# Performance work log

Hardware: AMD Instinct MI355X
Metric: run time of the kernel (lower is better)

The kernel has to match this reference:

```python
import jax, jax.numpy as jnp
import numpy as np

B, H, Q, N = 4, 32, 16, 4096
H_KV, D = 8, 128
N_KEEP = 3072
GROUPS = H // H_KV  # num_key_value_groups = 4


def setup_inputs() -> dict:
    key = jax.random.key(0)
    k1, k2, k3, k4 = jax.random.split(key, 4)
    attn_w = jax.random.uniform(k1, (B, H, Q, N), dtype=jnp.float32)
    # normalize to look like softmax output over the kv axis
    attn_w = attn_w / attn_w.sum(-1, keepdims=True)
    v_cache = jax.random.normal(k2, (B, H_KV, N, D), dtype=jnp.float32)
    o_proj_w = jax.random.normal(k3, (H * D, H * D), dtype=jnp.float32) * (1.0 / np.sqrt(H * D))
    keep_idx = jnp.sort(jax.random.randint(k4, (N_KEEP,), 0, N, dtype=jnp.int64))
    return {"attn_w": attn_w, "v_cache": v_cache, "o_proj_w": o_proj_w, "keep_idx": keep_idx}


def reference(attn_w, v_cache, o_proj_w, keep_idx):
    # 1) gather kept KV positions in the attention weights and renormalize
    aw = jnp.take(attn_w, keep_idx, axis=-1)              # [B,H,Q,Nk]
    aw = aw / (aw.sum(-1, keepdims=True) + 1e-6)
    # 2) gather kept V entries and repeat_kv across query-head groups
    v_new = jnp.take(v_cache, keep_idx, axis=2)           # [B,H_kv,Nk,D]
    v_all = jnp.repeat(v_new, GROUPS, axis=1)             # [B,H,Nk,D]
    # 3) recompute context and output projection
    ctx = jnp.einsum('bhqn,bhnd->bhqd', aw, v_all)        # [B,H,Q,D]
    ctx = ctx.transpose(0, 2, 1, 3).reshape(B, Q, H * D)  # [B,Q,H*D]
    out = ctx @ o_proj_w.T                                # nn.Linear: x @ W^T
    return out, aw
```

## Files before the change

### kernel.cpp

```cpp
#include <hip/hip_runtime.h>
#include <hip/hip_bf16.h>

#define BB   4
#define HH   32
#define QQ   16
#define NN   4096
#define HKV  8
#define DD   128
#define NK   3072
#define GRP  4

typedef __attribute__((ext_vector_type(8))) short bf16x8;
typedef __attribute__((ext_vector_type(4))) float f32x4;

__device__ __forceinline__ unsigned int pack_bf16(float lo, float hi) {
    union { unsigned int u; __hip_bfloat16 h[2]; } p;
    p.h[0] = __float2bfloat16(lo);
    p.h[1] = __float2bfloat16(hi);
    return p.u;
}

__global__ __launch_bounds__(256)
void k1_gather_norm(const float* __restrict__ attn_w,
                    const int* __restrict__ keep_idx,
                    float* __restrict__ aw_out)
{
    const int row = blockIdx.x;
    const float* src = attn_w + (size_t)row * NN;
    float* dst = aw_out + (size_t)row * NK;

    __shared__ float vals[NK];
    __shared__ float red[256];

    float s = 0.f;
    for (int k = threadIdx.x; k < NK; k += 256) {
        float v = src[keep_idx[k]];
        vals[k] = v;
        s += v;
    }
    red[threadIdx.x] = s;
    __syncthreads();
    for (int st = 128; st > 0; st >>= 1) {
        if (threadIdx.x < st) red[threadIdx.x] += red[threadIdx.x + st];
        __syncthreads();
    }
    const float inv = 1.0f / (red[0] + 1e-6f);
    for (int k = threadIdx.x; k < NK; k += 256)
        dst[k] = vals[k] * inv;
}

#define SPLITK2 16
#define KPB2    (NK / SPLITK2)
#define KCH     64

__global__ __launch_bounds__(256)
void k2_ctx(const float* __restrict__ aw,
            const float* __restrict__ v_cache,
            const int* __restrict__ keep_idx,
            __hip_bfloat16* __restrict__ partial)
{
    const int bid = blockIdx.x;
    const int ks  = bid & 15;
    const int hkv = (bid >> 4) & 7;
    const int b   = bid >> 7;
    const int tid = threadIdx.x;
    const int lane = tid & 63;
    const int w    = tid >> 6;
    const int fr   = lane & 15;
    const int kg   = lane >> 4;

    __shared__ unsigned short Vt[128 * 64];
    __shared__ int idxs[KCH];

    const int k0 = ks * KPB2;
    const float* arow = aw + (size_t)((b * HH + hkv * GRP + w) * QQ + fr) * NK + k0;
    const float* vb   = v_cache + (size_t)(b * HKV + hkv) * NN * DD;

    f32x4 acc[8];
#pragma unroll
    for (int nt = 0; nt < 8; ++nt) acc[nt] = (f32x4){0.f, 0.f, 0.f, 0.f};

    const int sd  = tid & 127;
    const int sc0 = tid >> 7;

    for (int c = 0; c < KPB2; c += KCH) {
        __syncthreads();
        if (tid < KCH) idxs[tid] = keep_idx[k0 + c + tid];
        __syncthreads();

#pragma unroll
        for (int p = 0; p < 4; ++p) {
            const int cs = sc0 + 2 * p;
            float v[8];
#pragma unroll
            for (int e = 0; e < 8; ++e)
                v[e] = vb[(size_t)idxs[8 * cs + e] * DD + sd];
            uint4 pk;
            pk.x = pack_bf16(v[0], v[1]);
            pk.y = pack_bf16(v[2], v[3]);
            pk.z = pack_bf16(v[4], v[5]);
            pk.w = pack_bf16(v[6], v[7]);
            const int us = sd * 64 + ((cs ^ (sd & 7)) << 3);
            *reinterpret_cast<uint4*>(&Vt[us]) = pk;
        }
        __syncthreads();

#pragma unroll
        for (int kc = 0; kc < 2; ++kc) {
            const float* ap = arow + c + kc * 32 + kg * 8;
            const float4 a0 = *reinterpret_cast<const float4*>(ap);
            const float4 a1 = *reinterpret_cast<const float4*>(ap + 4);
            union { bf16x8 v; unsigned int u[4]; } af;
            af.u[0] = pack_bf16(a0.x, a0.y);
            af.u[1] = pack_bf16(a0.z, a0.w);
            af.u[2] = pack_bf16(a1.x, a1.y);
            af.u[3] = pack_bf16(a1.z, a1.w);

            const int cs = kc * 4 + kg;
            const int xr = (cs ^ (fr & 7)) << 3;
#pragma unroll
            for (int nt = 0; nt < 8; ++nt) {
                const int d  = nt * 16 + fr;
                const int us = d * 64 + xr;
                bf16x8 bf = *reinterpret_cast<const bf16x8*>(&Vt[us]);
                acc[nt] = __builtin_amdgcn_mfma_f32_16x16x32_bf16(af.v, bf, acc[nt], 0, 0, 0);
            }
        }
    }

    __hip_bfloat16* pb = partial + (size_t)bid * (64 * DD);
#pragma unroll
    for (int nt = 0; nt < 8; ++nt) {
#pragma unroll
        for (int reg = 0; reg < 4; ++reg) {
            const int row = w * 16 + kg * 4 + reg;
            pb[row * DD + nt * 16 + fr] = __float2bfloat16(acc[nt][reg]);
        }
    }
}

__global__ __launch_bounds__(256)
void k3_reduce(const __hip_bfloat16* __restrict__ partial,
               __hip_bfloat16* __restrict__ ctxb)
{
    const int flat = blockIdx.x * 256 + threadIdx.x;
    const int bq = flat >> 12;
    const int i  = flat & 4095;
    const int b = bq >> 4, q = bq & 15;
    const int h = i >> 7,  d = i & 127;
    const int hkv = h >> 2, g = h & 3;
    const int r = g * 16 + q;

    const __hip_bfloat16* p = partial
        + (size_t)((b * 8 + hkv) * SPLITK2) * (64 * DD) + r * DD + d;
    float s = 0.f;
#pragma unroll
    for (int ss = 0; ss < SPLITK2; ++ss)
        s += __bfloat162float(p[(size_t)ss * (64 * DD)]);
    ctxb[flat] = __float2bfloat16(s);
}

#define K4SPLIT 8
#define K4LEN   (4096 / K4SPLIT)
#define KC4     128
#define LPAD    136

__global__ __launch_bounds__(256)
void k4_gemm(const __hip_bfloat16* __restrict__ ctxb,
             const float* __restrict__ W,
             float* __restrict__ pout)
{
    const int nt  = blockIdx.x >> 3;
    const int ks  = blockIdx.x & 7;
    const int tid = threadIdx.x;
    const int lane = tid & 63;
    const int w    = tid >> 6;

    __shared__ unsigned short Al[64][LPAD];
    __shared__ unsigned short Bl[32][LPAD];

    f32x4 acc0 = {0.f, 0.f, 0.f, 0.f};
    f32x4 acc1 = {0.f, 0.f, 0.f, 0.f};

    const unsigned short* ctxu = reinterpret_cast<const unsigned short*>(ctxb);
    const int kbase = ks * K4LEN;
    const int fr = lane & 15;
    const int kg = lane >> 4;

    for (int ch = 0; ch < K4LEN / KC4; ++ch) {
        const int kb = kbase + ch * KC4;
        __syncthreads();

        {
            const int cc = tid & 15;
            const int r0 = tid >> 4;
#pragma unroll
            for (int p = 0; p < 4; ++p) {
                const int r = r0 + p * 16;
                float4 v = *reinterpret_cast<const float4*>(
                    ctxu + (size_t)r * 4096 + kb + cc * 8);
                *reinterpret_cast<float4*>(&Al[r][cc * 8]) = v;
            }
        }
        {
            const int cc = tid & 31;
            const int r0 = tid >> 5;
#pragma unroll
            for (int p = 0; p < 4; ++p) {
                const int r = r0 + p * 8;
                float4 v = *reinterpret_cast<const float4*>(
                    W + (size_t)(nt * 32 + r) * 4096 + kb + cc * 4);
                union { ushort4 u; __hip_bfloat16 h[4]; } pk;
                pk.h[0] = __float2bfloat16(v.x);
                pk.h[1] = __float2bfloat16(v.y);
                pk.h[2] = __float2bfloat16(v.z);
                pk.h[3] = __float2bfloat16(v.w);
                *reinterpret_cast<ushort4*>(&Bl[r][cc * 4]) = pk.u;
            }
        }
        __syncthreads();

#pragma unroll
        for (int kst = 0; kst < KC4 / 32; ++kst) {
            const int ko = kst * 32 + kg * 8;
            bf16x8 a  = *reinterpret_cast<const bf16x8*>(&Al[w * 16 + fr][ko]);
            bf16x8 b0 = *reinterpret_cast<const bf16x8*>(&Bl[fr][ko]);
            bf16x8 b1 = *reinterpret_cast<const bf16x8*>(&Bl[16 + fr][ko]);
            acc0 = __builtin_amdgcn_mfma_f32_16x16x32_bf16(a, b0, acc0, 0, 0, 0);
            acc1 = __builtin_amdgcn_mfma_f32_16x16x32_bf16(a, b1, acc1, 0, 0, 0);
        }
    }

    float* pb = pout + (size_t)ks * (64 * 4096);
#pragma unroll
    for (int reg = 0; reg < 4; ++reg) {
        const int row = w * 16 + kg * 4 + reg;
        pb[(size_t)row * 4096 + nt * 32 + fr]      = acc0[reg];
        pb[(size_t)row * 4096 + nt * 32 + 16 + fr] = acc1[reg];
    }
}

__global__ __launch_bounds__(256)
void k5_out(const float* __restrict__ pout, float* __restrict__ out)
{
    const int flat = blockIdx.x * 256 + threadIdx.x;
    float s = 0.f;
#pragma unroll
    for (int ss = 0; ss < K4SPLIT; ++ss)
        s += pout[(size_t)ss * (64 * 4096) + flat];
    out[flat] = s;
}

extern "C" void kernel_launch(void* const* d_in, const int* in_sizes, int n_in,
                              void* d_out, int out_size, void* d_ws, size_t ws_size,
                              hipStream_t stream)
{
    const float* attn_w  = (const float*)d_in[0];
    const float* v_cache = (const float*)d_in[1];
    const float* o_proj  = (const float*)d_in[2];
    const int*   keep_idx = (const int*)d_in[3];

    float* out    = (float*)d_out;
    float* aw_out = (float*)d_out + 262144;

    __hip_bfloat16* partial2 = (__hip_bfloat16*)d_ws;
    __hip_bfloat16* ctxb = (__hip_bfloat16*)((char*)d_ws + (size_t)8 * 1024 * 1024);
    float* pout = (float*)d_ws;

    k1_gather_norm<<<BB * HH * QQ, 256, 0, stream>>>(attn_w, keep_idx, aw_out);
    k2_ctx<<<BB * HKV * SPLITK2, 256, 0, stream>>>(aw_out, v_cache, keep_idx, partial2);
    k3_reduce<<<(64 * 4096) / 256, 256, 0, stream>>>(partial2, ctxb);
    k4_gemm<<<128 * K4SPLIT, 256, 0, stream>>>(ctxb, o_proj, pout);
    k5_out<<<(64 * 4096) / 256, 256, 0, stream>>>(pout, out);
}
```

Before: 48.88 us.

## Emit bf16 weights from gather, widen ctx blocks, store GEMM partials in bf16

The gather/normalize kernel now also writes a bf16 copy of the renormalized weights, so the context kernel loads bf16 A fragments directly instead of converting from fp32. The context kernel runs 512 threads per block, splitting the D dimension across two wave halves with fewer accumulators each, which halves the per-thread V staging work. The output GEMM's split-K partials are stored as bf16 instead of fp32, halving partial-buffer traffic for the GEMM and the final reduce. This costs some accuracy in the split-K sum and adds an extra bf16 write in the first kernel.

```diff
diff --git a/kernel.cpp b/kernel.cpp
--- a/kernel.cpp
+++ b/kernel.cpp
@@ -23,11 +23,13 @@
 __global__ __launch_bounds__(256)
 void k1_gather_norm(const float* __restrict__ attn_w,
                     const int* __restrict__ keep_idx,
-                    float* __restrict__ aw_out)
+                    float* __restrict__ aw_out,
+                    __hip_bfloat16* __restrict__ aw16)
 {
     const int row = blockIdx.x;
     const float* src = attn_w + (size_t)row * NN;
     float* dst = aw_out + (size_t)row * NK;
+    unsigned int* dst16 = reinterpret_cast<unsigned int*>(aw16 + (size_t)row * NK);
 
     __shared__ float vals[NK];
     __shared__ float red[256];
@@ -45,16 +47,20 @@
         __syncthreads();
     }
     const float inv = 1.0f / (red[0] + 1e-6f);
-    for (int k = threadIdx.x; k < NK; k += 256)
-        dst[k] = vals[k] * inv;
+    for (int k = threadIdx.x * 2; k < NK; k += 512) {
+        float a = vals[k] * inv;
+        float b = vals[k + 1] * inv;
+        *reinterpret_cast<float2*>(&dst[k]) = make_float2(a, b);
+        dst16[k >> 1] = pack_bf16(a, b);
+    }
 }
 
 #define SPLITK2 16
 #define KPB2    (NK / SPLITK2)
 #define KCH     64
 
-__global__ __launch_bounds__(256)
-void k2_ctx(const float* __restrict__ aw,
+__global__ __launch_bounds__(512, 4)
+void k2_ctx(const __hip_bfloat16* __restrict__ aw16,
             const float* __restrict__ v_cache,
             const int* __restrict__ keep_idx,
             __hip_bfloat16* __restrict__ partial)
@@ -66,6 +72,8 @@
     const int tid = threadIdx.x;
     const int lane = tid & 63;
     const int w    = tid >> 6;
+    const int mw   = w & 3;
+    const int nh   = w >> 2;
     const int fr   = lane & 15;
     const int kg   = lane >> 4;
 
@@ -73,12 +81,13 @@
     __shared__ int idxs[KCH];
 
     const int k0 = ks * KPB2;
-    const float* arow = aw + (size_t)((b * HH + hkv * GRP + w) * QQ + fr) * NK + k0;
-    const float* vb   = v_cache + (size_t)(b * HKV + hkv) * NN * DD;
-
-    f32x4 acc[8];
-#pragma unroll
-    for (int nt = 0; nt < 8; ++nt) acc[nt] = (f32x4){0.f, 0.f, 0.f, 0.f};
+    const unsigned short* arow = reinterpret_cast<const unsigned short*>(aw16)
+        + (size_t)((b * HH + hkv * GRP + mw) * QQ + fr) * NK + k0;
+    const float* vb = v_cache + (size_t)(b * HKV + hkv) * NN * DD;
+
+    f32x4 acc[4];
+#pragma unroll
+    for (int nt = 0; nt < 4; ++nt) acc[nt] = (f32x4){0.f, 0.f, 0.f, 0.f};
 
     const int sd  = tid & 127;
     const int sc0 = tid >> 7;
@@ -89,8 +98,8 @@
         __syncthreads();
 
 #pragma unroll
-        for (int p = 0; p < 4; ++p) {
-            const int cs = sc0 + 2 * p;
+        for (int p = 0; p < 2; ++p) {
+            const int cs = sc0 + 4 * p;
             float v[8];
 #pragma unroll
             for (int e = 0; e < 8; ++e)
@@ -107,34 +116,26 @@
 
 #pragma unroll
         for (int kc = 0; kc < 2; ++kc) {
-            const float* ap = arow + c + kc * 32 + kg * 8;
-            const float4 a0 = *reinterpret_cast<const float4*>(ap);
-            const float4 a1 = *reinterpret_cast<const float4*>(ap + 4);
-            union { bf16x8 v; unsigned int u[4]; } af;
-            af.u[0] = pack_bf16(a0.x, a0.y);
-            af.u[1] = pack_bf16(a0.z, a0.w);
-            af.u[2] = pack_bf16(a1.x, a1.y);
-            af.u[3] = pack_bf16(a1.z, a1.w);
-
+            bf16x8 af = *reinterpret_cast<const bf16x8*>(arow + c + kc * 32 + kg * 8);
             const int cs = kc * 4 + kg;
             const int xr = (cs ^ (fr & 7)) << 3;
 #pragma unroll
-            for (int nt = 0; nt < 8; ++nt) {
-                const int d  = nt * 16 + fr;
+            for (int nt = 0; nt < 4; ++nt) {
+                const int d  = (nh * 4 + nt) * 16 + fr;
                 const int us = d * 64 + xr;
                 bf16x8 bf = *reinterpret_cast<const bf16x8*>(&Vt[us]);
-                acc[nt] = __builtin_amdgcn_mfma_f32_16x16x32_bf16(af.v, bf, acc[nt], 0, 0, 0);
+                acc[nt] = __builtin_amdgcn_mfma_f32_16x16x32_bf16(af, bf, acc[nt], 0, 0, 0);
             }
         }
     }
 
     __hip_bfloat16* pb = partial + (size_t)bid * (64 * DD);
 #pragma unroll
-    for (int nt = 0; nt < 8; ++nt) {
+    for (int nt = 0; nt < 4; ++nt) {
 #pragma unroll
         for (int reg = 0; reg < 4; ++reg) {
-            const int row = w * 16 + kg * 4 + reg;
-            pb[row * DD + nt * 16 + fr] = __float2bfloat16(acc[nt][reg]);
+            const int row = mw * 16 + kg * 4 + reg;
+            pb[row * DD + (nh * 4 + nt) * 16 + fr] = __float2bfloat16(acc[nt][reg]);
         }
     }
 }
@@ -165,10 +166,10 @@
 #define KC4     128
 #define LPAD    136
 
-__global__ __launch_bounds__(256)
+__global__ __launch_bounds__(256, 4)
 void k4_gemm(const __hip_bfloat16* __restrict__ ctxb,
              const float* __restrict__ W,
-             float* __restrict__ pout)
+             __hip_bfloat16* __restrict__ pout)
 {
     const int nt  = blockIdx.x >> 3;
     const int ks  = blockIdx.x & 7;
@@ -231,23 +232,23 @@
         }
     }
 
-    float* pb = pout + (size_t)ks * (64 * 4096);
+    __hip_bfloat16* pb = pout + (size_t)ks * (64 * 4096);
 #pragma unroll
     for (int reg = 0; reg < 4; ++reg) {
         const int row = w * 16 + kg * 4 + reg;
-        pb[(size_t)row * 4096 + nt * 32 + fr]      = acc0[reg];
-        pb[(size_t)row * 4096 + nt * 32 + 16 + fr] = acc1[reg];
+        pb[(size_t)row * 4096 + nt * 32 + fr]      = __float2bfloat16(acc0[reg]);
+        pb[(size_t)row * 4096 + nt * 32 + 16 + fr] = __float2bfloat16(acc1[reg]);
     }
 }
 
 __global__ __launch_bounds__(256)
-void k5_out(const float* __restrict__ pout, float* __restrict__ out)
+void k5_out(const __hip_bfloat16* __restrict__ pout, float* __restrict__ out)
 {
     const int flat = blockIdx.x * 256 + threadIdx.x;
     float s = 0.f;
 #pragma unroll
     for (int ss = 0; ss < K4SPLIT; ++ss)
-        s += pout[(size_t)ss * (64 * 4096) + flat];
+        s += __bfloat162float(pout[(size_t)ss * (64 * 4096) + flat]);
     out[flat] = s;
 }
 
@@ -265,10 +266,11 @@
 
     __hip_bfloat16* partial2 = (__hip_bfloat16*)d_ws;
     __hip_bfloat16* ctxb = (__hip_bfloat16*)((char*)d_ws + (size_t)8 * 1024 * 1024);
-    float* pout = (float*)d_ws;
-
-    k1_gather_norm<<<BB * HH * QQ, 256, 0, stream>>>(attn_w, keep_idx, aw_out);
-    k2_ctx<<<BB * HKV * SPLITK2, 256, 0, stream>>>(aw_out, v_cache, keep_idx, partial2);
+    __hip_bfloat16* aw16 = (__hip_bfloat16*)((char*)d_ws + (size_t)9 * 1024 * 1024);
+    __hip_bfloat16* pout = (__hip_bfloat16*)d_ws;
+
+    k1_gather_norm<<<BB * HH * QQ, 256, 0, stream>>>(attn_w, keep_idx, aw_out, aw16);
+    k2_ctx<<<BB * HKV * SPLITK2, 512, 0, stream>>>(aw16, v_cache, keep_idx, partial2);
     k3_reduce<<<(64 * 4096) / 256, 256, 0, stream>>>(partial2, ctxb);
     k4_gemm<<<128 * K4SPLIT, 256, 0, stream>>>(ctxb, o_proj, pout);
     k5_out<<<(64 * 4096) / 256, 256, 0, stream>>>(pout, out);
```

Result: no change. 48.47 us (median of 2 runs) (-0.8%).

## Replace split-K GEMM plus reduce kernel with in-block K-split reduction

Applied to the files above, without the earlier changes.

The output projection GEMM no longer writes 8 split-K partial slabs to workspace and runs a separate reduction kernel. Each 512-thread block now covers 16 output columns, and its two wave groups handle the two K halves over the full 4096-wide K range. The halves are summed through shared memory and written straight to the output, removing one launch and the partial-sum round trip through global memory. The grid shrinks to 256 blocks that each do more serial K work, and the gather/normalize store is also widened to float2.

```diff
diff --git a/kernel.cpp b/kernel.cpp
--- a/kernel.cpp
+++ b/kernel.cpp
@@ -45,8 +45,11 @@
         __syncthreads();
     }
     const float inv = 1.0f / (red[0] + 1e-6f);
-    for (int k = threadIdx.x; k < NK; k += 256)
-        dst[k] = vals[k] * inv;
+    for (int k = threadIdx.x * 2; k < NK; k += 512) {
+        float a = vals[k] * inv;
+        float b = vals[k + 1] * inv;
+        *reinterpret_cast<float2*>(&dst[k]) = make_float2(a, b);
+    }
 }
 
 #define SPLITK2 16
@@ -160,95 +163,84 @@
     ctxb[flat] = __float2bfloat16(s);
 }
 
-#define K4SPLIT 8
-#define K4LEN   (4096 / K4SPLIT)
-#define KC4     128
-#define LPAD    136
-
-__global__ __launch_bounds__(256)
+#define KH4  2048
+#define KC4  128
+#define LPAD 136
+
+__global__ __launch_bounds__(512, 2)
 void k4_gemm(const __hip_bfloat16* __restrict__ ctxb,
              const float* __restrict__ W,
-             float* __restrict__ pout)
-{
-    const int nt  = blockIdx.x >> 3;
-    const int ks  = blockIdx.x & 7;
+             float* __restrict__ out)
+{
+    const int nt  = blockIdx.x;
     const int tid = threadIdx.x;
     const int lane = tid & 63;
     const int w    = tid >> 6;
-
-    __shared__ unsigned short Al[64][LPAD];
-    __shared__ unsigned short Bl[32][LPAD];
-
-    f32x4 acc0 = {0.f, 0.f, 0.f, 0.f};
-    f32x4 acc1 = {0.f, 0.f, 0.f, 0.f};
+    const int mw   = w & 3;
+    const int kh   = w >> 2;
+    const int fr   = lane & 15;
+    const int kg   = lane >> 4;
+
+    __shared__ unsigned short Al[2][64][LPAD];
+    __shared__ unsigned short Bl[2][16][LPAD];
+    __shared__ float Rt[4][16][16];
 
     const unsigned short* ctxu = reinterpret_cast<const unsigned short*>(ctxb);
-    const int kbase = ks * K4LEN;
-    const int fr = lane & 15;
-    const int kg = lane >> 4;
-
-    for (int ch = 0; ch < K4LEN / KC4; ++ch) {
-        const int kb = kbase + ch * KC4;
-        __syncthreads();
-
-        {
-            const int cc = tid & 15;
-            const int r0 = tid >> 4;
-#pragma unroll
-            for (int p = 0; p < 4; ++p) {
-                const int r = r0 + p * 16;
-                float4 v = *reinterpret_cast<const float4*>(
-                    ctxu + (size_t)r * 4096 + kb + cc * 8);
-                *reinterpret_cast<float4*>(&Al[r][cc * 8]) = v;
-            }
-        }
-        {
-            const int cc = tid & 31;
-            const int r0 = tid >> 5;
-#pragma unroll
-            for (int p = 0; p < 4; ++p) {
-                const int r = r0 + p * 8;
-                float4 v = *reinterpret_cast<const float4*>(
-                    W + (size_t)(nt * 32 + r) * 4096 + kb + cc * 4);
-                union { ushort4 u; __hip_bfloat16 h[4]; } pk;
-                pk.h[0] = __float2bfloat16(v.x);
-                pk.h[1] = __float2bfloat16(v.y);
-                pk.h[2] = __float2bfloat16(v.z);
-                pk.h[3] = __float2bfloat16(v.w);
-                *reinterpret_cast<ushort4*>(&Bl[r][cc * 4]) = pk.u;
-            }
-        }
-        __syncthreads();
-
-#pragma unroll
-        for (int kst = 0; kst < KC4 / 32; ++kst) {
-            const int ko = kst * 32 + kg * 8;
-            bf16x8 a  = *reinterpret_cast<const bf16x8*>(&Al[w * 16 + fr][ko]);
-            bf16x8 b0 = *reinterpret_cast<const bf16x8*>(&Bl[fr][ko]);
-            bf16x8 b1 = *reinterpret_cast<const bf16x8*>(&Bl[16 + fr][ko]);
-            acc0 = __builtin_amdgcn_mfma_f32_16x16x32_bf16(a, b0, acc0, 0, 0, 0);
-            acc1 = __builtin_amdgcn_mfma_f32_16x16x32_bf16(a, b1, acc1, 0, 0, 0);
-        }
-    }
-
-    float* pb = pout + (size_t)ks * (64 * 4096);
-#pragma unroll
-    for (int reg = 0; reg < 4; ++reg) {
-        const int row = w * 16 + kg * 4 + reg;
-        pb[(size_t)row * 4096 + nt * 32 + fr]      = acc0[reg];
-        pb[(size_t)row * 4096 + nt * 32 + 16 + fr] = acc1[reg];
-    }
-}
-
-__global__ __launch_bounds__(256)
-void k5_out(const float* __restrict__ pout, float* __restrict__ out)
-{
-    const int flat = blockIdx.x * 256 + threadIdx.x;
-    float s = 0.f;
-#pragma unroll
-    for (int ss = 0; ss < K4SPLIT; ++ss)
-        s += pout[(size_t)ss * (64 * 4096) + flat];
-    out[flat] = s;
+    f32x4 acc = {0.f, 0.f, 0.f, 0.f};
+
+    for (int i = 0; i < 16; ++i) {
+        __syncthreads();
+
+#pragma unroll
+        for (int p = 0; p < 4; ++p) {
+            const int u  = tid + 512 * p;
+            const int c8 = u & 15;
+            const int r  = (u >> 4) & 63;
+            const int ah = u >> 10;
+            *reinterpret_cast<float4*>(&Al[ah][r][c8 * 8]) =
+                *reinterpret_cast<const float4*>(
+                    ctxu + (size_t)r * 4096 + ah * KH4 + i * KC4 + c8 * 8);
+        }
+#pragma unroll
+        for (int p = 0; p < 2; ++p) {
+            const int u  = tid + 512 * p;
+            const int cc = u & 31;
+            const int r  = (u >> 5) & 15;
+            const int bh = u >> 9;
+            float4 v = *reinterpret_cast<const float4*>(
+                W + (size_t)(nt * 16 + r) * 4096 + bh * KH4 + i * KC4 + cc * 4);
+            union { ushort4 u4; __hip_bfloat16 h[4]; } pk;
+            pk.h[0] = __float2bfloat16(v.x);
+            pk.h[1] = __float2bfloat16(v.y);
+            pk.h[2] = __float2bfloat16(v.z);
+            pk.h[3] = __float2bfloat16(v.w);
+            *reinterpret_cast<ushort4*>(&Bl[bh][r][cc * 4]) = pk.u4;
+        }
+        __syncthreads();
+
+#pragma unroll
+        for (int kc = 0; kc < 4; ++kc) {
+            const int ko = kc * 32 + kg * 8;
+            bf16x8 a  = *reinterpret_cast<const bf16x8*>(&Al[kh][mw * 16 + fr][ko]);
+            bf16x8 bv = *reinterpret_cast<const bf16x8*>(&Bl[kh][fr][ko]);
+            acc = __builtin_amdgcn_mfma_f32_16x16x32_bf16(a, bv, acc, 0, 0, 0);
+        }
+    }
+
+    __syncthreads();
+    if (kh == 1) {
+#pragma unroll
+        for (int reg = 0; reg < 4; ++reg)
+            Rt[mw][kg * 4 + reg][fr] = acc[reg];
+    }
+    __syncthreads();
+    if (kh == 0) {
+#pragma unroll
+        for (int reg = 0; reg < 4; ++reg) {
+            const int bq = mw * 16 + kg * 4 + reg;
+            out[(size_t)bq * 4096 + nt * 16 + fr] = acc[reg] + Rt[mw][kg * 4 + reg][fr];
+        }
+    }
 }
 
 extern "C" void kernel_launch(void* const* d_in, const int* in_sizes, int n_in,
@@ -265,11 +257,9 @@
 
     __hip_bfloat16* partial2 = (__hip_bfloat16*)d_ws;
     __hip_bfloat16* ctxb = (__hip_bfloat16*)((char*)d_ws + (size_t)8 * 1024 * 1024);
-    float* pout = (float*)d_ws;
 
     k1_gather_norm<<<BB * HH * QQ, 256, 0, stream>>>(attn_w, keep_idx, aw_out);
     k2_ctx<<<BB * HKV * SPLITK2, 256, 0, stream>>>(aw_out, v_cache, keep_idx, partial2);
     k3_reduce<<<(64 * 4096) / 256, 256, 0, stream>>>(partial2, ctxb);
-    k4_gemm<<<128 * K4SPLIT, 256, 0, stream>>>(ctxb, o_proj, pout);
-    k5_out<<<(64 * 4096) / 256, 256, 0, stream>>>(pout, out);
-}
+    k4_gemm<<<256, 512, 0, stream>>>(ctxb, o_proj, out);
+}
```

After: 56.33 us. +15.2%, slower.
